# Kernel tuning notes

Measured on AMD Instinct MI355X. Metric: run time of the kernel, lower is better.

The kernel has to match this reference:

```python
import jax, jax.numpy as jnp
import numpy as np

Q_DIM = 256; KV_DIM = 256; C = 32; N_HEAD = 8; OUT_DIM = 256
B1, B2, LQ, LK = 1, 128, 256, 256


def _glorot(key, shape, gain=1.0):
    fan_in, fan_out = shape[-2], shape[-1]
    std = gain * np.sqrt(2.0 / float(fan_in + fan_out))
    dev = np.sqrt(3.0) * std
    return jax.random.uniform(key, shape, jnp.float32, -dev, dev)


def setup_inputs() -> dict:
    key = jax.random.key(0)
    ks = jax.random.split(key, 12)
    q_data = jax.random.normal(ks[0], (B1, B2, LQ, Q_DIM), jnp.float32)
    kv_data = jax.random.normal(ks[1], (B1, B2, LK, KV_DIM), jnp.float32)
    bias = jax.random.normal(ks[2], (B1, B2, N_HEAD, LQ, LK), jnp.float32)
    nonbatched_bias = jax.random.normal(ks[3], (B1, N_HEAD, LQ, LK), jnp.float32)
    # torch Linear weights are [out, in]; original init is zeros but we use
    # glorot for a non-degenerate numerical baseline.
    Wq = _glorot(ks[4], (N_HEAD * C, Q_DIM))
    Wk = _glorot(ks[5], (N_HEAD * C, KV_DIM))
    Wv = _glorot(ks[6], (N_HEAD * C, KV_DIM))
    Wg = _glorot(ks[7], (N_HEAD * C, Q_DIM))
    bg = jnp.ones((N_HEAD * C,), jnp.float32)  # bias_init=1.0
    Wo = _glorot(ks[8], (OUT_DIM, N_HEAD * C))
    bo = jnp.zeros((OUT_DIM,), jnp.float32)
    return dict(q_data=q_data, kv_data=kv_data, bias=bias,
                nonbatched_bias=nonbatched_bias, Wq=Wq, Wk=Wk, Wv=Wv,
                Wg=Wg, bg=bg, Wo=Wo, bo=bo)


def reference(q_data, kv_data, bias, nonbatched_bias, Wq, Wk, Wv, Wg, bg, Wo, bo):
    c = C
    # projections: [b1,b2,len,n_head,c]
    q = (q_data @ Wq.T).reshape(*q_data.shape[:-1], N_HEAD, c) * (c ** -0.5)
    k = (kv_data @ Wk.T).reshape(*kv_data.shape[:-1], N_HEAD, c)
    v = (kv_data @ Wv.T).reshape(*kv_data.shape[:-1], N_HEAD, c)
    # logits: [b1,b2,n_head,len_q,len_kv]
    logits = jnp.einsum('bsqhc,bskhc->bshqk', q, k)
    logits = logits + bias + nonbatched_bias[:, None]
    weights = jax.nn.softmax(logits, axis=-1)
    weighted_avg = jnp.einsum('bshqk,bskhc->bsqhc', weights, v)
    gate = jax.nn.sigmoid((q_data @ Wg.T + bg).reshape(*q_data.shape[:-1], N_HEAD, c))
    weighted_avg = weighted_avg * gate
    out = weighted_avg.reshape(*weighted_avg.shape[:-2], N_HEAD * c) @ Wo.T + bo
    return out
```

## Files before the change

### kernel.cpp

```cpp
#include <hip/hip_runtime.h>
#include <hip/hip_bf16.h>

#define NB2 128
#define LQK 256
#define DIM 256
#define NH 8
#define CC 32

typedef __bf16 bf16x8 __attribute__((ext_vector_type(8)));
typedef __bf16 bf16x4 __attribute__((ext_vector_type(4)));
typedef float f32x4 __attribute__((ext_vector_type(4)));

#define MFMA16 __builtin_amdgcn_mfma_f32_16x16x32_bf16

#define TP 72

#define NTOK ((size_t)NB2 * LQK * NH * CC)

static __device__ __forceinline__ void gload_lds16(const void* g, void* l) {
    __builtin_amdgcn_global_load_lds(
        (const __attribute__((address_space(1))) unsigned int*)g,
        (__attribute__((address_space(3))) unsigned int*)l,
        16, 0, 0);
}

__global__ __launch_bounds__(256) void k_wcvt(
    const float* __restrict__ Wq, const float* __restrict__ Wk,
    const float* __restrict__ Wv, const float* __restrict__ Wg,
    const float* __restrict__ Wo, __bf16* __restrict__ dst)
{
    int i = (blockIdx.x * 256 + threadIdx.x) * 4;
    int mat = i >> 16;
    int off = i & 65535;
    const float* src = (mat == 0) ? Wq : (mat == 1) ? Wk : (mat == 2) ? Wv
                      : (mat == 3) ? Wg : Wo;
    f32x4 v = *(const f32x4*)(src + off);
    __bf16* d = dst + ((size_t)mat << 16) + off;
    d[0] = (__bf16)v[0]; d[1] = (__bf16)v[1]; d[2] = (__bf16)v[2]; d[3] = (__bf16)v[3];
}

__global__ __launch_bounds__(256) void k_acvt(
    const float* __restrict__ qd, const float* __restrict__ kvd,
    __bf16* __restrict__ qbf, __bf16* __restrict__ kvbf)
{
    size_t i = ((size_t)blockIdx.x * 256 + threadIdx.x) * 8;
    const float* src;
    __bf16* dst;
    if (i < NTOK) { src = qd + i; dst = qbf + i; }
    else          { src = kvd + (i - NTOK); dst = kvbf + (i - NTOK); }
    f32x4 a = *(const f32x4*)src;
    f32x4 b = *(const f32x4*)(src + 4);
    bf16x8 r;
    r[0] = (__bf16)a[0]; r[1] = (__bf16)a[1]; r[2] = (__bf16)a[2]; r[3] = (__bf16)a[3];
    r[4] = (__bf16)b[0]; r[5] = (__bf16)b[1]; r[6] = (__bf16)b[2]; r[7] = (__bf16)b[3];
    *(bf16x8*)dst = r;
}

__global__ __launch_bounds__(256, 2) void k_proj(
    const __bf16* __restrict__ qbf, const __bf16* __restrict__ kvbf,
    const __bf16* __restrict__ wBF, const float* __restrict__ bg,
    __bf16* __restrict__ wsq, __bf16* __restrict__ wsk,
    __bf16* __restrict__ wsvT, __bf16* __restrict__ wsgT)
{
    __shared__ __bf16 At[2][128][TP];
    __shared__ __bf16 Bt[2][128][TP];

    const int mb = blockIdx.x, nb = blockIdx.y;
    const int t = nb >> 1;
    const __bf16* X = (t == 0 || t == 3) ? qbf : kvbf;
    const __bf16* W = wBF + ((size_t)t << 16) + (size_t)((nb & 1) * 128) * 256;

    const int tid = threadIdx.x;
    const int lane = tid & 63, w = tid >> 6;
    const int g = lane >> 4, kg = g * 8, c0 = lane & 15;
    const int mq = (w >> 1) * 64, nq = (w & 1) * 64;
    const int m0 = mb * 128;
    const int srow = tid >> 1, shalf = (tid & 1) * 32;

    f32x4 acc[4][4] = {};
    bf16x8 av[4], bv[4];
    auto load_stage = [&](int kit) {
        const __bf16* ap = X + (size_t)(m0 + srow) * DIM + kit * 64 + shalf;
        const __bf16* bp = W + (size_t)srow * 256 + kit * 64 + shalf;
#pragma unroll
        for (int j = 0; j < 4; j++) {
            av[j] = *(const bf16x8*)(ap + j * 8);
            bv[j] = *(const bf16x8*)(bp + j * 8);
        }
    };
    auto write_stage = [&](int buf) {
#pragma unroll
        for (int j = 0; j < 4; j++) {
            *(bf16x8*)(&At[buf][srow][shalf + j * 8]) = av[j];
            *(bf16x8*)(&Bt[buf][srow][shalf + j * 8]) = bv[j];
        }
    };

    load_stage(0);
    write_stage(0);
    __syncthreads();

#pragma unroll
    for (int kit = 0; kit < 4; kit++) {
        if (kit < 3) load_stage(kit + 1);
        const int cur = kit & 1;
#pragma unroll
        for (int ks = 0; ks < 2; ks++) {
            bf16x8 af[4], bf_[4];
#pragma unroll
            for (int mi = 0; mi < 4; mi++)
                af[mi] = *(const bf16x8*)(&At[cur][mq + mi * 16 + c0][ks * 32 + kg]);
#pragma unroll
            for (int ni = 0; ni < 4; ni++)
                bf_[ni] = *(const bf16x8*)(&Bt[cur][nq + ni * 16 + c0][ks * 32 + kg]);
#pragma unroll
            for (int mi = 0; mi < 4; mi++)
#pragma unroll
                for (int ni = 0; ni < 4; ni++)
                    acc[mi][ni] = MFMA16(af[mi], bf_[ni], acc[mi][ni], 0, 0, 0);
        }
        if (kit < 3) write_stage(cur ^ 1);
        __syncthreads();
    }

#pragma unroll
    for (int ni = 0; ni < 4; ni++) {
        const int nloc = (nb & 1) * 128 + nq + ni * 16 + c0;
        const int h = nloc >> 5, c = nloc & 31;
        const float bg_ = (t == 3) ? bg[nloc] : 0.0f;
#pragma unroll
        for (int mi = 0; mi < 4; mi++) {
            const int mbase = m0 + mq + mi * 16 + g * 4;
            const int b2 = mbase >> 8;
            if (t == 2) {
                bf16x4 pk;
#pragma unroll
                for (int reg = 0; reg < 4; reg++) pk[reg] = (__bf16)acc[mi][ni][reg];
                *(bf16x4*)(&wsvT[((size_t)(b2 * NH + h) * CC + c) * LQK + (mbase & 255)]) = pk;
            } else if (t == 3) {
                bf16x4 pk;
#pragma unroll
                for (int reg = 0; reg < 4; reg++)
                    pk[reg] = (__bf16)(1.0f / (1.0f + __expf(-(acc[mi][ni][reg] + bg_))));
                *(bf16x4*)(&wsgT[((size_t)(b2 * NH + h) * CC + c) * LQK + (mbase & 255)]) = pk;
            } else {
#pragma unroll
                for (int reg = 0; reg < 4; reg++) {
                    const int l = (mbase + reg) & 255;
                    float v = acc[mi][ni][reg];
                    size_t idx = ((size_t)(b2 * NH + h) * LQK + l) * CC + c;
                    if (t == 0) wsq[idx] = (__bf16)(v * 0.17677669529663689f);
                    else        wsk[idx] = (__bf16)v;
                }
            }
        }
    }
}

__global__ __launch_bounds__(256, 2) void k_attn(
    const __bf16* __restrict__ wsq, const __bf16* __restrict__ wsk,
    const __bf16* __restrict__ wsvT, const __bf16* __restrict__ wsgT,
    const float* __restrict__ bias, const float* __restrict__ nbb,
    __bf16* __restrict__ wswa)
{
    __shared__ float  Bl[2][64][64];
    __shared__ __bf16 Kl[2][2048];
    __shared__ __bf16 Vl[2][2048];
    __shared__ __bf16 P[4][16][TP];

    const int tid = threadIdx.x;
    const int u0 = blockIdx.x;
    const int xcd = u0 & 7, slot = u0 >> 3;
    const int head = xcd + 8 * (slot >> 2);
    const int qt = slot & 3;
    const int b2 = head >> 3, h = head & 7;

    const int lane = tid & 63, w = tid >> 6;
    const int g = lane >> 4, kg = g * 8, c0 = lane & 15;
    const int qbase = qt * 64 + w * 16;
    const int q = qbase + c0;
    const int rw = w * 16 + c0;

    const __bf16* qp = wsq + (size_t)(b2 * NH + h) * LQK * CC;
    const __bf16* kp = wsk + (size_t)(b2 * NH + h) * LQK * CC;
    const __bf16* vT = wsvT + (size_t)(b2 * NH + h) * CC * LQK;
    const __bf16* gT = wsgT + (size_t)(b2 * NH + h) * CC * LQK;
    const float* np = nbb + ((size_t)h * LQK + q) * LQK;
    const float* bblk = bias + ((size_t)(b2 * NH + h) * LQK + qt * 64) * LQK;

    auto stage = [&](int buf, int c) {
        const int rbase = tid >> 4, jj = tid & 15;
#pragma unroll
        for (int i = 0; i < 4; i++) {
            const int row = i * 16 + rbase;
            const int uu = jj ^ (row & 7);
            gload_lds16(bblk + (size_t)row * LQK + c * 64 + uu * 4,
                        &Bl[buf][i * 16 + w * 4][0]);
        }
        {
            const int su = (lane & 3) ^ ((lane >> 3) & 3);
            gload_lds16(kp + (size_t)(c * 64 + w * 16 + (lane >> 2)) * CC + su * 8,
                        &Kl[buf][w * 512]);
        }
        {
            const int su = (lane & 7) ^ (lane >> 3);
            gload_lds16(vT + (size_t)(w * 8 + (lane >> 3)) * LQK + c * 64 + su * 8,
                        &Vl[buf][w * 512]);
        }
    };

    bf16x8 qf = *(const bf16x8*)(qp + (size_t)q * CC + kg);

    stage(0, 0);
    __syncthreads();

    float l = 0.0f;
    f32x4 o[2] = {};

#pragma unroll
    for (int c = 0; c < 4; c++) {
        const int cur = c & 1;
        if (c < 3) stage(cur ^ 1, c + 1);

        float csum = 0.0f;
#pragma unroll
        for (int j = 0; j < 4; j++) {
            const int su = ((j * 4 + g) ^ (rw & 7)) * 4;
            f32x4 b4 = *(const f32x4*)(&Bl[cur][rw][su]);
            f32x4 n4 = *(const f32x4*)(np + c * 64 + j * 16 + g * 4);
            bf16x8 kf = *(const bf16x8*)(
                &Kl[cur][((j * 16 + c0) * 4 + (g ^ ((c0 >> 1) & 3))) * 8]);
            f32x4 cc;
#pragma unroll
            for (int r2 = 0; r2 < 4; r2++) cc[r2] = b4[r2] + n4[r2];
            f32x4 s = MFMA16(kf, qf, cc, 0, 0, 0);
            bf16x4 pk;
#pragma unroll
            for (int r2 = 0; r2 < 4; r2++) {
                float e = __expf(s[r2]);
                csum += e;
                pk[r2] = (__bf16)e;
            }
            *(bf16x4*)(&P[w][c0][j * 16 + g * 4]) = pk;
        }
        l += csum;
#pragma unroll
        for (int kt2 = 0; kt2 < 2; kt2++) {
            bf16x8 pa = *(const bf16x8*)(&P[w][c0][kt2 * 32 + kg]);
#pragma unroll
            for (int vn = 0; vn < 2; vn++) {
                bf16x8 vb = *(const bf16x8*)(
                    &Vl[cur][((vn * 16 + c0) * 8 + ((kt2 * 4 + g) ^ (c0 & 7))) * 8]);
                o[vn] = MFMA16(pa, vb, o[vn], 0, 0, 0);
            }
        }
        if (c < 3) __syncthreads();
    }

    l += __shfl_xor(l, 16);
    l += __shfl_xor(l, 32);
    const float inv = 1.0f / l;

#pragma unroll
    for (int vn = 0; vn < 2; vn++) {
        const int c = vn * 16 + c0;
        bf16x4 g4 = *(const bf16x4*)(gT + (size_t)c * LQK + qbase + g * 4);
#pragma unroll
        for (int reg = 0; reg < 4; reg++) {
            const int row = qbase + g * 4 + reg;
            const float invr = __shfl(inv, g * 4 + reg, 64);
            const float val = o[vn][reg] * invr * (float)g4[reg];
            wswa[((size_t)(b2 * LQK + row)) * (NH * CC) + h * CC + c] = (__bf16)val;
        }
    }
}

__global__ __launch_bounds__(256, 2) void k_out(
    const __bf16* __restrict__ wa, const __bf16* __restrict__ wBF,
    const float* __restrict__ bo, float* __restrict__ out)
{
    __shared__ __bf16 At[2][128][TP];
    __shared__ __bf16 Bt[2][128][TP];

    const int mb = blockIdx.x, nb = blockIdx.y;
    const __bf16* W = wBF + ((size_t)4 << 16) + (size_t)(nb * 128) * 256;

    const int tid = threadIdx.x;
    const int lane = tid & 63, w = tid >> 6;
    const int g = lane >> 4, kg = g * 8, c0 = lane & 15;
    const int mq = (w >> 1) * 64, nq = (w & 1) * 64;
    const int m0 = mb * 128;
    const int srow = tid >> 1, shalf = (tid & 1) * 32;

    f32x4 acc[4][4] = {};
    bf16x8 av[4], bv[4];
    auto load_stage = [&](int kit) {
        const __bf16* ap = wa + (size_t)(m0 + srow) * 256 + kit * 64 + shalf;
        const __bf16* bp = W + (size_t)srow * 256 + kit * 64 + shalf;
#pragma unroll
        for (int j = 0; j < 4; j++) {
            av[j] = *(const bf16x8*)(ap + j * 8);
            bv[j] = *(const bf16x8*)(bp + j * 8);
        }
    };
    auto write_stage = [&](int buf) {
#pragma unroll
        for (int j = 0; j < 4; j++) {
            *(bf16x8*)(&At[buf][srow][shalf + j * 8]) = av[j];
            *(bf16x8*)(&Bt[buf][srow][shalf + j * 8]) = bv[j];
        }
    };

    load_stage(0);
    write_stage(0);
    __syncthreads();

#pragma unroll
    for (int kit = 0; kit < 4; kit++) {
        if (kit < 3) load_stage(kit + 1);
        const int cur = kit & 1;
#pragma unroll
        for (int ks = 0; ks < 2; ks++) {
            bf16x8 af[4], bf_[4];
#pragma unroll
            for (int mi = 0; mi < 4; mi++)
                af[mi] = *(const bf16x8*)(&At[cur][mq + mi * 16 + c0][ks * 32 + kg]);
#pragma unroll
            for (int ni = 0; ni < 4; ni++)
                bf_[ni] = *(const bf16x8*)(&Bt[cur][nq + ni * 16 + c0][ks * 32 + kg]);
#pragma unroll
            for (int mi = 0; mi < 4; mi++)
#pragma unroll
                for (int ni = 0; ni < 4; ni++)
                    acc[mi][ni] = MFMA16(af[mi], bf_[ni], acc[mi][ni], 0, 0, 0);
        }
        if (kit < 3) write_stage(cur ^ 1);
        __syncthreads();
    }

#pragma unroll
    for (int ni = 0; ni < 4; ni++) {
        const int n = nb * 128 + nq + ni * 16 + c0;
        const float bo_ = bo[n];
#pragma unroll
        for (int mi = 0; mi < 4; mi++) {
            const int mbase = m0 + mq + mi * 16 + g * 4;
#pragma unroll
            for (int reg = 0; reg < 4; reg++)
                out[(size_t)(mbase + reg) * 256 + n] = acc[mi][ni][reg] + bo_;
        }
    }
}

extern "C" void kernel_launch(void* const* d_in, const int* in_sizes, int n_in,
                              void* d_out, int out_size, void* d_ws, size_t ws_size,
                              hipStream_t stream) {
    const float* qd  = (const float*)d_in[0];
    const float* kvd = (const float*)d_in[1];
    const float* bias = (const float*)d_in[2];
    const float* nbb = (const float*)d_in[3];
    const float* Wq = (const float*)d_in[4];
    const float* Wk = (const float*)d_in[5];
    const float* Wv = (const float*)d_in[6];
    const float* Wg = (const float*)d_in[7];
    const float* bg = (const float*)d_in[8];
    const float* Wo = (const float*)d_in[9];
    const float* bo = (const float*)d_in[10];
    float* out = (float*)d_out;

    __bf16* ws = (__bf16*)d_ws;
    __bf16* wsq  = ws;
    __bf16* wsk  = wsq + NTOK;
    __bf16* wsvT = wsk + NTOK;
    __bf16* wsgT = wsvT + NTOK;
    __bf16* wBF  = wsgT + NTOK;
    __bf16* qbf  = wBF + 5 * 65536;
    __bf16* kvbf = qbf + NTOK;
    __bf16* wswa = qbf;

    k_wcvt<<<dim3(320), 256, 0, stream>>>(Wq, Wk, Wv, Wg, Wo, wBF);
    k_acvt<<<dim3(8192), 256, 0, stream>>>(qd, kvd, qbf, kvbf);
    k_proj<<<dim3(256, 8), 256, 0, stream>>>(qbf, kvbf, wBF, bg,
                                             wsq, wsk, wsvT, wsgT);
    k_attn<<<dim3(4096), 256, 0, stream>>>(wsq, wsk, wsvT, wsgT, bias, nbb, wswa);
    k_out<<<dim3(256, 2), 256, 0, stream>>>(wswa, wBF, bo, out);
}
```

Measured before the change: 165.5 us.

## Triple-buffer attention staging with explicit vmcnt waits and preload nonbatched bias

Changes k_attn from double to triple buffering of the bias, K and V tiles. Barriers now use explicit s_waitcnt vmcnt counts, so two stages stay in flight while a tile is computed. The nonbatched-bias row is preloaded into 16 registers up front instead of being fetched from global memory inside the loop. The P scratch is shrunk so the P·V MFMA runs per 32-key half, which limits its LDS footprint. The cost is extra LDS, roughly 64KB for three buffers, which may cut occupancy below two blocks per CU. It also adds register pressure and hand-counted waitcnt values that must match the number of loads issued per stage.

```diff
diff --git a/kernel.cpp b/kernel.cpp
--- a/kernel.cpp
+++ b/kernel.cpp
@@ -23,6 +23,11 @@
         (__attribute__((address_space(3))) unsigned int*)l,
         16, 0, 0);
 }
+
+#define WAITV(N) do { asm volatile("s_waitcnt vmcnt(" #N ")" ::: "memory"); \
+                      __builtin_amdgcn_sched_barrier(0); } while (0)
+#define BARRIER() do { __builtin_amdgcn_s_barrier(); \
+                       __builtin_amdgcn_sched_barrier(0); } while (0)
 
 __global__ __launch_bounds__(256) void k_wcvt(
     const float* __restrict__ Wq, const float* __restrict__ Wk,
@@ -163,10 +168,10 @@
     const float* __restrict__ bias, const float* __restrict__ nbb,
     __bf16* __restrict__ wswa)
 {
-    __shared__ float  Bl[2][64][64];
-    __shared__ __bf16 Kl[2][2048];
-    __shared__ __bf16 Vl[2][2048];
-    __shared__ __bf16 P[4][16][TP];
+    __shared__ float  Bl[3][64][64];
+    __shared__ __bf16 Kl[3][2048];
+    __shared__ __bf16 Vl[3][2048];
+    __shared__ __bf16 Ps[4][16][34];
 
     const int tid = threadIdx.x;
     const int u0 = blockIdx.x;
@@ -188,6 +193,15 @@
     const float* np = nbb + ((size_t)h * LQK + q) * LQK;
     const float* bblk = bias + ((size_t)(b2 * NH + h) * LQK + qt * 64) * LQK;
 
+    bf16x8 qf = *(const bf16x8*)(qp + (size_t)q * CC + kg);
+    f32x4 nb[16];
+#pragma unroll
+    for (int t = 0; t < 16; t++) nb[t] = *(const f32x4*)(np + t * 16 + g * 4);
+    asm volatile("" : "+v"(qf));
+#pragma unroll
+    for (int t = 0; t < 16; t++) asm volatile("" : "+v"(nb[t]));
+    __builtin_amdgcn_sched_barrier(0);
+
     auto stage = [&](int buf, int c) {
         const int rbase = tid >> 4, jj = tid & 15;
 #pragma unroll
@@ -209,53 +223,61 @@
         }
     };
 
-    bf16x8 qf = *(const bf16x8*)(qp + (size_t)q * CC + kg);
-
-    stage(0, 0);
-    __syncthreads();
-
     float l = 0.0f;
     f32x4 o[2] = {};
 
-#pragma unroll
-    for (int c = 0; c < 4; c++) {
-        const int cur = c & 1;
-        if (c < 3) stage(cur ^ 1, c + 1);
-
+    auto compute = [&](int buf, int c) {
         float csum = 0.0f;
 #pragma unroll
-        for (int j = 0; j < 4; j++) {
-            const int su = ((j * 4 + g) ^ (rw & 7)) * 4;
-            f32x4 b4 = *(const f32x4*)(&Bl[cur][rw][su]);
-            f32x4 n4 = *(const f32x4*)(np + c * 64 + j * 16 + g * 4);
-            bf16x8 kf = *(const bf16x8*)(
-                &Kl[cur][((j * 16 + c0) * 4 + (g ^ ((c0 >> 1) & 3))) * 8]);
-            f32x4 cc;
-#pragma unroll
-            for (int r2 = 0; r2 < 4; r2++) cc[r2] = b4[r2] + n4[r2];
-            f32x4 s = MFMA16(kf, qf, cc, 0, 0, 0);
-            bf16x4 pk;
-#pragma unroll
-            for (int r2 = 0; r2 < 4; r2++) {
-                float e = __expf(s[r2]);
-                csum += e;
-                pk[r2] = (__bf16)e;
+        for (int h2 = 0; h2 < 2; h2++) {
+#pragma unroll
+            for (int jj2 = 0; jj2 < 2; jj2++) {
+                const int j = h2 * 2 + jj2;
+                const int su = ((j * 4 + g) ^ (rw & 7)) * 4;
+                f32x4 b4 = *(const f32x4*)(&Bl[buf][rw][su]);
+                bf16x8 kf = *(const bf16x8*)(
+                    &Kl[buf][((j * 16 + c0) * 4 + (g ^ ((c0 >> 1) & 3))) * 8]);
+                f32x4 cc;
+                const f32x4 n4 = nb[c * 4 + j];
+#pragma unroll
+                for (int r2 = 0; r2 < 4; r2++) cc[r2] = b4[r2] + n4[r2];
+                f32x4 s = MFMA16(kf, qf, cc, 0, 0, 0);
+                bf16x4 pk;
+#pragma unroll
+                for (int r2 = 0; r2 < 4; r2++) {
+                    float e = __expf(s[r2]);
+                    csum += e;
+                    pk[r2] = (__bf16)e;
+                }
+                *(bf16x4*)(&Ps[w][c0][jj2 * 16 + g * 4]) = pk;
             }
-            *(bf16x4*)(&P[w][c0][j * 16 + g * 4]) = pk;
-        }
-        l += csum;
-#pragma unroll
-        for (int kt2 = 0; kt2 < 2; kt2++) {
-            bf16x8 pa = *(const bf16x8*)(&P[w][c0][kt2 * 32 + kg]);
+            bf16x8 pa = *(const bf16x8*)(&Ps[w][c0][kg]);
 #pragma unroll
             for (int vn = 0; vn < 2; vn++) {
                 bf16x8 vb = *(const bf16x8*)(
-                    &Vl[cur][((vn * 16 + c0) * 8 + ((kt2 * 4 + g) ^ (c0 & 7))) * 8]);
+                    &Vl[buf][((vn * 16 + c0) * 8 + ((h2 * 4 + g) ^ (c0 & 7))) * 8]);
                 o[vn] = MFMA16(pa, vb, o[vn], 0, 0, 0);
             }
         }
-        if (c < 3) __syncthreads();
-    }
+        l += csum;
+    };
+
+    stage(0, 0);
+    stage(1, 1);
+
+    WAITV(6);  BARRIER();
+    stage(2, 2);
+    compute(0, 0);
+
+    WAITV(6);  BARRIER();
+    stage(0, 3);
+    compute(1, 1);
+
+    WAITV(6);  BARRIER();
+    compute(2, 2);
+
+    WAITV(0);  BARRIER();
+    compute(0, 3);
 
     l += __shfl_xor(l, 16);
     l += __shfl_xor(l, 32);
```

After: 167.9 us. Within noise of the previous version (+1.4%).

## Load V directly to registers in attention, merge convert kernels, raise occupancy

Applied to the files above, without the earlier changes.

The attention kernel stops staging V through LDS. Each lane now loads its V fragments and the non-batched bias straight from global memory into registers at the top of each chunk, with scheduling barriers so these loads are issued ahead of the async staging. This frees LDS, and launch bounds are raised to allow three blocks per CU. The two fp32-to-bf16 conversion kernels are merged into one launch to save a kernel launch, at the cost of more register pressure and uncoalesced per-lane V reads.

```diff
diff --git a/kernel.cpp b/kernel.cpp
--- a/kernel.cpp
+++ b/kernel.cpp
@@ -24,36 +24,37 @@
         16, 0, 0);
 }
 
-__global__ __launch_bounds__(256) void k_wcvt(
+__global__ __launch_bounds__(256) void k_cvt(
+    const float* __restrict__ qd, const float* __restrict__ kvd,
     const float* __restrict__ Wq, const float* __restrict__ Wk,
     const float* __restrict__ Wv, const float* __restrict__ Wg,
-    const float* __restrict__ Wo, __bf16* __restrict__ dst)
+    const float* __restrict__ Wo,
+    __bf16* __restrict__ qbf, __bf16* __restrict__ kvbf,
+    __bf16* __restrict__ wBF)
 {
-    int i = (blockIdx.x * 256 + threadIdx.x) * 4;
-    int mat = i >> 16;
-    int off = i & 65535;
-    const float* src = (mat == 0) ? Wq : (mat == 1) ? Wk : (mat == 2) ? Wv
-                      : (mat == 3) ? Wg : Wo;
-    f32x4 v = *(const f32x4*)(src + off);
-    __bf16* d = dst + ((size_t)mat << 16) + off;
-    d[0] = (__bf16)v[0]; d[1] = (__bf16)v[1]; d[2] = (__bf16)v[2]; d[3] = (__bf16)v[3];
-}
-
-__global__ __launch_bounds__(256) void k_acvt(
-    const float* __restrict__ qd, const float* __restrict__ kvd,
-    __bf16* __restrict__ qbf, __bf16* __restrict__ kvbf)
-{
-    size_t i = ((size_t)blockIdx.x * 256 + threadIdx.x) * 8;
-    const float* src;
-    __bf16* dst;
-    if (i < NTOK) { src = qd + i; dst = qbf + i; }
-    else          { src = kvd + (i - NTOK); dst = kvbf + (i - NTOK); }
-    f32x4 a = *(const f32x4*)src;
-    f32x4 b = *(const f32x4*)(src + 4);
-    bf16x8 r;
-    r[0] = (__bf16)a[0]; r[1] = (__bf16)a[1]; r[2] = (__bf16)a[2]; r[3] = (__bf16)a[3];
-    r[4] = (__bf16)b[0]; r[5] = (__bf16)b[1]; r[6] = (__bf16)b[2]; r[7] = (__bf16)b[3];
-    *(bf16x8*)dst = r;
+    const int b = blockIdx.x;
+    if (b < 8192) {
+        size_t i = ((size_t)b * 256 + threadIdx.x) * 8;
+        const float* src;
+        __bf16* dst;
+        if (i < NTOK) { src = qd + i; dst = qbf + i; }
+        else          { src = kvd + (i - NTOK); dst = kvbf + (i - NTOK); }
+        f32x4 a = *(const f32x4*)src;
+        f32x4 c = *(const f32x4*)(src + 4);
+        bf16x8 r;
+        r[0] = (__bf16)a[0]; r[1] = (__bf16)a[1]; r[2] = (__bf16)a[2]; r[3] = (__bf16)a[3];
+        r[4] = (__bf16)c[0]; r[5] = (__bf16)c[1]; r[6] = (__bf16)c[2]; r[7] = (__bf16)c[3];
+        *(bf16x8*)dst = r;
+    } else {
+        int i = ((b - 8192) * 256 + threadIdx.x) * 4;
+        int mat = i >> 16;
+        int off = i & 65535;
+        const float* src = (mat == 0) ? Wq : (mat == 1) ? Wk : (mat == 2) ? Wv
+                          : (mat == 3) ? Wg : Wo;
+        f32x4 v = *(const f32x4*)(src + off);
+        __bf16* d = wBF + ((size_t)mat << 16) + off;
+        d[0] = (__bf16)v[0]; d[1] = (__bf16)v[1]; d[2] = (__bf16)v[2]; d[3] = (__bf16)v[3];
+    }
 }
 
 __global__ __launch_bounds__(256, 2) void k_proj(
@@ -157,7 +158,7 @@
     }
 }
 
-__global__ __launch_bounds__(256, 2) void k_attn(
+__global__ __launch_bounds__(256, 3) void k_attn(
     const __bf16* __restrict__ wsq, const __bf16* __restrict__ wsk,
     const __bf16* __restrict__ wsvT, const __bf16* __restrict__ wsgT,
     const float* __restrict__ bias, const float* __restrict__ nbb,
@@ -165,7 +166,6 @@
 {
     __shared__ float  Bl[2][64][64];
     __shared__ __bf16 Kl[2][2048];
-    __shared__ __bf16 Vl[2][2048];
     __shared__ __bf16 P[4][16][TP];
 
     const int tid = threadIdx.x;
@@ -202,11 +202,6 @@
             gload_lds16(kp + (size_t)(c * 64 + w * 16 + (lane >> 2)) * CC + su * 8,
                         &Kl[buf][w * 512]);
         }
-        {
-            const int su = (lane & 7) ^ (lane >> 3);
-            gload_lds16(vT + (size_t)(w * 8 + (lane >> 3)) * LQK + c * 64 + su * 8,
-                        &Vl[buf][w * 512]);
-        }
     };
 
     bf16x8 qf = *(const bf16x8*)(qp + (size_t)q * CC + kg);
@@ -220,19 +215,33 @@
 #pragma unroll
     for (int c = 0; c < 4; c++) {
         const int cur = c & 1;
+
+        bf16x8 vf[4];
+        f32x4 n4[4];
+#pragma unroll
+        for (int kt2 = 0; kt2 < 2; kt2++)
+#pragma unroll
+            for (int vn = 0; vn < 2; vn++)
+                vf[kt2 * 2 + vn] = *(const bf16x8*)(
+                    vT + (size_t)(vn * 16 + c0) * LQK + c * 64 + kt2 * 32 + kg);
+#pragma unroll
+        for (int j = 0; j < 4; j++)
+            n4[j] = *(const f32x4*)(np + c * 64 + j * 16 + g * 4);
+        __builtin_amdgcn_sched_barrier(0);
+
         if (c < 3) stage(cur ^ 1, c + 1);
+        __builtin_amdgcn_sched_barrier(0);
 
         float csum = 0.0f;
 #pragma unroll
         for (int j = 0; j < 4; j++) {
             const int su = ((j * 4 + g) ^ (rw & 7)) * 4;
             f32x4 b4 = *(const f32x4*)(&Bl[cur][rw][su]);
-            f32x4 n4 = *(const f32x4*)(np + c * 64 + j * 16 + g * 4);
             bf16x8 kf = *(const bf16x8*)(
                 &Kl[cur][((j * 16 + c0) * 4 + (g ^ ((c0 >> 1) & 3))) * 8]);
             f32x4 cc;
 #pragma unroll
-            for (int r2 = 0; r2 < 4; r2++) cc[r2] = b4[r2] + n4[r2];
+            for (int r2 = 0; r2 < 4; r2++) cc[r2] = b4[r2] + n4[j][r2];
             f32x4 s = MFMA16(kf, qf, cc, 0, 0, 0);
             bf16x4 pk;
 #pragma unroll
@@ -248,11 +257,8 @@
         for (int kt2 = 0; kt2 < 2; kt2++) {
             bf16x8 pa = *(const bf16x8*)(&P[w][c0][kt2 * 32 + kg]);
 #pragma unroll
-            for (int vn = 0; vn < 2; vn++) {
-                bf16x8 vb = *(const bf16x8*)(
-                    &Vl[cur][((vn * 16 + c0) * 8 + ((kt2 * 4 + g) ^ (c0 & 7))) * 8]);
-                o[vn] = MFMA16(pa, vb, o[vn], 0, 0, 0);
-            }
+            for (int vn = 0; vn < 2; vn++)
+                o[vn] = MFMA16(pa, vf[kt2 * 2 + vn], o[vn], 0, 0, 0);
         }
         if (c < 3) __syncthreads();
     }
@@ -378,8 +384,8 @@
     __bf16* kvbf = qbf + NTOK;
     __bf16* wswa = qbf;
 
-    k_wcvt<<<dim3(320), 256, 0, stream>>>(Wq, Wk, Wv, Wg, Wo, wBF);
-    k_acvt<<<dim3(8192), 256, 0, stream>>>(qd, kvd, qbf, kvbf);
+    k_cvt<<<dim3(8512), 256, 0, stream>>>(qd, kvd, Wq, Wk, Wv, Wg, Wo,
+                                          qbf, kvbf, wBF);
     k_proj<<<dim3(256, 8), 256, 0, stream>>>(qbf, kvbf, wBF, bg,
                                              wsq, wsk, wsvT, wsgT);
     k_attn<<<dim3(4096), 256, 0, stream>>>(wsq, wsk, wsvT, wsgT, bias, nbb, wswa);
```

After: 168.5 us. About the same (+1.8%).
